# Kernel optimization log

Measured on AMD Instinct MI355X. Metric: run time of the kernel, lower is better.

Reference implementation:

```python
import jax, jax.numpy as jnp
import numpy as np

B, S, E, H = 4, 2048, 256, 8  # batch, seq_len, embed_dim, depth (heads)


def setup_inputs() -> dict:
    key = jax.random.key(0)
    k_x, k_q, k_k, k_v = jax.random.split(key, 4)
    return {
        "x": jax.random.normal(k_x, (B, S, E), dtype=jnp.float32),
        "w_q": jax.random.normal(k_q, (H, E, E), dtype=jnp.float32),
        "w_k": jax.random.normal(k_k, (H, E, E), dtype=jnp.float32),
        "w_v": jax.random.normal(k_v, (H, E, E), dtype=jnp.float32),
    }


def reference(x, w_q, w_k, w_v):
    # Each head uses full embed_dim projections; heads are averaged at the end.
    embed_dim = x.shape[-1]
    scale = 1.0 / np.sqrt(embed_dim).astype(np.float32)
    q = jnp.einsum("bse,hef->bhsf", x, w_q)  # [B,H,S,E]
    k = jnp.einsum("bse,hef->bhsf", x, w_k)
    v = jnp.einsum("bse,hef->bhsf", x, w_v)
    scores = jax.nn.softmax(jnp.einsum("bhsf,bhtf->bhst", q, k) * scale, axis=-1)
    out = jnp.einsum("bhst,bhtf->bhsf", scores, v)  # [B,H,S,E]
    return out.mean(axis=1)  # [B,S,E]
```

## Files before the change

kernel.cpp:

```cpp
#include <hip/hip_runtime.h>
#include <hip/hip_bf16.h>
#include <cstdint>

#define B_N 4
#define S_N 2048
#define E_N 256
#define H_N 8

typedef float f32x4 __attribute__((ext_vector_type(4)));
typedef int i32x4 __attribute__((ext_vector_type(4)));
typedef short s16x8 __attribute__((ext_vector_type(8)));

static __device__ __forceinline__ f32x4 mfma16(s16x8 a, s16x8 b, f32x4 c) {
  return __builtin_amdgcn_mfma_f32_16x16x32_bf16(a, b, c, 0, 0, 0);
}
static __device__ __forceinline__ i32x4 mfma8i(i32x4 a, i32x4 b, i32x4 c) {
  return __builtin_amdgcn_mfma_i32_16x16x64_i8(a, b, c, 0, 0, 0);
}

static __device__ __forceinline__ unsigned short f2bf(float f) {
  union { float f; unsigned int u; } v; v.f = f;
  unsigned int r = v.u + 0x7fffu + ((v.u >> 16) & 1u);
  return (unsigned short)(r >> 16);
}
static __device__ __forceinline__ float bf2f(unsigned short s) {
  union { unsigned int u; float f; } v; v.u = ((unsigned int)s) << 16;
  return v.f;
}
static __device__ __forceinline__ unsigned short f2bf_fast(float f) {
  __hip_bfloat16 h = __float2bfloat16(f);
  return *(unsigned short*)&h;
}

static __device__ __forceinline__ void limbs(float v, float scale, int& hi8, int& lo8) {
  int x = (int)lrintf(v * scale);
  x = x < -32639 ? -32639 : (x > 32639 ? 32639 : x);
  hi8 = (x + 128) >> 8;
  lo8 = x - (hi8 << 8);
}

static __device__ __forceinline__ void gload16(const void* g, void* l) {
  __builtin_amdgcn_global_load_lds(
      (const __attribute__((address_space(1))) unsigned int*)g,
      (__attribute__((address_space(3))) unsigned int*)l, 16, 0, 0);
}

static __device__ __forceinline__ float dppmax16(float x) {
  x = fmaxf(x, __int_as_float(__builtin_amdgcn_update_dpp(
          0, __float_as_int(x), 0xB1, 0xF, 0xF, true)));
  x = fmaxf(x, __int_as_float(__builtin_amdgcn_update_dpp(
          0, __float_as_int(x), 0x4E, 0xF, 0xF, true)));
  x = fmaxf(x, __int_as_float(__builtin_amdgcn_update_dpp(
          0, __float_as_int(x), 0x141, 0xF, 0xF, true)));
  x = fmaxf(x, __int_as_float(__builtin_amdgcn_update_dpp(
          0, __float_as_int(x), 0x140, 0xF, 0xF, true)));
  return x;
}
static __device__ __forceinline__ float dppsum16(float x) {
  x = x + __int_as_float(__builtin_amdgcn_update_dpp(
          0, __float_as_int(x), 0xB1, 0xF, 0xF, true));
  x = x + __int_as_float(__builtin_amdgcn_update_dpp(
          0, __float_as_int(x), 0x4E, 0xF, 0xF, true));
  x = x + __int_as_float(__builtin_amdgcn_update_dpp(
          0, __float_as_int(x), 0x141, 0xF, 0xF, true));
  x = x + __int_as_float(__builtin_amdgcn_update_dpp(
          0, __float_as_int(x), 0x140, 0xF, 0xF, true));
  return x;
}

__global__ void k_split(const float* __restrict__ src, unsigned short* __restrict__ hi,
                        unsigned short* __restrict__ lo, int n4) {
  int i = blockIdx.x * blockDim.x + threadIdx.x;
  if (i >= n4) return;
  float4 v = ((const float4*)src)[i];
  float f[4] = {v.x, v.y, v.z, v.w};
  unsigned short hh[4], ll[4];
#pragma unroll
  for (int j = 0; j < 4; j++) {
    hh[j] = f2bf(f[j]);
    ll[j] = f2bf(f[j] - bf2f(hh[j]));
  }
  ushort4 h; h.x = hh[0]; h.y = hh[1]; h.z = hh[2]; h.w = hh[3];
  ushort4 l; l.x = ll[0]; l.y = ll[1]; l.z = ll[2]; l.w = ll[3];
  ((ushort4*)hi)[i] = h;
  ((ushort4*)lo)[i] = l;
}

__global__ void k_split8(const float* __restrict__ src, signed char* __restrict__ hi,
                         signed char* __restrict__ lo, int n4) {
  int i = blockIdx.x * blockDim.x + threadIdx.x;
  if (i >= n4) return;
  float4 v = ((const float4*)src)[i];
  float f[4] = {v.x, v.y, v.z, v.w};
  signed char hh[4], ll[4];
#pragma unroll
  for (int j = 0; j < 4; j++) {
    int h8, l8;
    limbs(f[j], 4096.f, h8, l8);
    hh[j] = (signed char)h8;
    ll[j] = (signed char)l8;
  }
  *(int*)(hi + i * 4) = *(int*)hh;
  *(int*)(lo + i * 4) = *(int*)ll;
}

__global__ void k_transpose_wv(const float* __restrict__ wv, unsigned short* __restrict__ wvT) {
  __shared__ float t[32][33];
  int h = blockIdx.z;
  int e0 = blockIdx.x * 32, f0 = blockIdx.y * 32;
  int tx = threadIdx.x & 31, ty = threadIdx.x >> 5;
  const float* src = wv + ((size_t)h * E_N + e0) * E_N + f0;
#pragma unroll
  for (int r = ty; r < 32; r += 8) t[r][tx] = src[(size_t)r * E_N + tx];
  __syncthreads();
  unsigned short* dst = wvT + ((size_t)h * E_N + f0) * E_N + e0;
#pragma unroll
  for (int r = ty; r < 32; r += 8) dst[(size_t)r * E_N + tx] = f2bf(t[tx][r]);
}

#define BKP 40

template <int TERMS, int OUT_MODE>
__global__ __launch_bounds__(256, 2) void k_gemm(
    const unsigned short* __restrict__ Ahi, const unsigned short* __restrict__ Alo,
    const unsigned short* __restrict__ Bhi, const unsigned short* __restrict__ Blo,
    unsigned short* __restrict__ Chi, unsigned short* __restrict__ Clo,
    int K, int N,
    int aDiv, int aMod, long long aStr,
    int bDiv, int bMod, long long bStr,
    long long cStr) {
  __shared__ unsigned short sA[2][128 * BKP];
  __shared__ unsigned short sB[2][128 * BKP];
  int z = blockIdx.z;
  const unsigned short* A0h = Ahi + (long long)((z / aDiv) % aMod) * aStr;
  const unsigned short* A0l = Alo + (long long)((z / aDiv) % aMod) * aStr;
  const unsigned short* B0h = Bhi + (long long)((z / bDiv) % bMod) * bStr;
  const unsigned short* B0l = Blo + (long long)((z / bDiv) % bMod) * bStr;
  int rT = blockIdx.x * 128, cT = blockIdx.y * 128;
  int tid = threadIdx.x;
  int w = tid >> 6, l = tid & 63, lr = l & 15, lg = l >> 4;
  int wr = w >> 1, wc = w & 1;

  f32x4 acc[4][4];
#pragma unroll
  for (int i = 0; i < 4; i++)
#pragma unroll
    for (int j = 0; j < 4; j++) acc[i][j] = (f32x4){0.f, 0.f, 0.f, 0.f};

  for (int k0 = 0; k0 < K; k0 += 32) {
#pragma unroll
    for (int it = 0; it < 2; it++) {
      int idx = (it * 256 + tid) * 8;
      int r = idx >> 5, c = idx & 31;
      *(s16x8*)&sA[0][r * BKP + c] = *(const s16x8*)(A0h + (size_t)(rT + r) * K + k0 + c);
      *(s16x8*)&sB[0][r * BKP + c] = *(const s16x8*)(B0h + (size_t)(cT + r) * K + k0 + c);
      if (TERMS == 3) {
        *(s16x8*)&sA[1][r * BKP + c] = *(const s16x8*)(A0l + (size_t)(rT + r) * K + k0 + c);
        *(s16x8*)&sB[1][r * BKP + c] = *(const s16x8*)(B0l + (size_t)(cT + r) * K + k0 + c);
      }
    }
    __syncthreads();
    s16x8 ah[4], al[4], bh[4], bl[4];
#pragma unroll
    for (int i = 0; i < 4; i++) {
      ah[i] = *(const s16x8*)&sA[0][(wr * 64 + i * 16 + lr) * BKP + lg * 8];
      if (TERMS == 3) al[i] = *(const s16x8*)&sA[1][(wr * 64 + i * 16 + lr) * BKP + lg * 8];
    }
#pragma unroll
    for (int j = 0; j < 4; j++) {
      bh[j] = *(const s16x8*)&sB[0][(wc * 64 + j * 16 + lr) * BKP + lg * 8];
      if (TERMS == 3) bl[j] = *(const s16x8*)&sB[1][(wc * 64 + j * 16 + lr) * BKP + lg * 8];
    }
#pragma unroll
    for (int i = 0; i < 4; i++)
#pragma unroll
      for (int j = 0; j < 4; j++) {
        acc[i][j] = mfma16(ah[i], bh[j], acc[i][j]);
        if (TERMS == 3) {
          acc[i][j] = mfma16(ah[i], bl[j], acc[i][j]);
          acc[i][j] = mfma16(al[i], bh[j], acc[i][j]);
        }
      }
    __syncthreads();
  }
  long long cOff = (long long)z * cStr;
#pragma unroll
  for (int i = 0; i < 4; i++)
#pragma unroll
    for (int j = 0; j < 4; j++)
#pragma unroll
      for (int r = 0; r < 4; r++) {
        int row = rT + wr * 64 + i * 16 + lg * 4 + r;
        int col = cT + wc * 64 + j * 16 + lr;
        float v = acc[i][j][r];
        long long e = cOff + (size_t)row * N + col;
        if (OUT_MODE == 2) {
          int h8, l8;
          limbs(v, 16.f, h8, l8);
          ((signed char*)Chi)[e] = (signed char)h8;
          ((signed char*)Clo)[e] = (signed char)l8;
        } else {
          unsigned short hb = f2bf(v);
          Chi[e] = hb;
          if (OUT_MODE == 1) Clo[e] = f2bf(v - bf2f(hb));
        }
      }
}

#define TT 64
#define BUFS 65536
#define ATTN_LDS 147456
#define THR 40.f

__global__ __launch_bounds__(512, 2) void k_attn(
    const signed char* __restrict__ Y8h, const signed char* __restrict__ Y8l,
    const signed char* __restrict__ X8h, const signed char* __restrict__ X8l,
    const unsigned short* __restrict__ VT, float* __restrict__ Out) {
  extern __shared__ char smem[];

  int obid = blockIdx.x;
  int swz = (obid & 7) * 64 + (obid >> 3);
  int qt = swz & 15, bh = swz >> 4;
  int b = bh >> 3;
  int tid = threadIdx.x, w = tid >> 6, l = tid & 63, lr = l & 15, lg = l >> 4;
  const signed char* Ybh_h = Y8h + (size_t)bh * (S_N * E_N);
  const signed char* Ybh_l = Y8l + (size_t)bh * (S_N * E_N);
  const signed char* Xb_h = X8h + (size_t)b * (S_N * E_N);
  const signed char* Xb_l = X8l + (size_t)b * (S_N * E_N);
  const unsigned short* Vbh = VT + (size_t)bh * (E_N * S_N);
  int qrow = qt * 128 + w * 16;

  int xs8[2];
#pragma unroll
  for (int i = 0; i < 2; i++) {
    int c = (w * 2 + i) * 64 + l;
    int t8 = c >> 4;
    xs8[i] = t8 * 256 + (((c & 15) ^ (t8 & 15)) * 16);
  }
  int vsrc[4];
#pragma unroll
  for (int i = 0; i < 4; i++) {
    int c = (w * 4 + i) * 64 + l;
    int vrow = c >> 3, vbyt = (c & 7) * 16;
    vsrc[i] = vrow * S_N + ((vbyt ^ ((vrow & 7) << 4)) >> 1);
  }

  int xrb[4];
#pragma unroll
  for (int kb = 0; kb < 4; kb++)
    xrb[kb] = lr * 256 + (((kb * 4 + lg) ^ lr) * 16);
  int vtb[2];
#pragma unroll
  for (int tc = 0; tc < 2; tc++)
    vtb[tc] = lr * 128 + ((tc * 64 + lg * 16) ^ ((lr & 7) << 4));
  int prb = 131072 + w * 2048 + lr * 128 + ((lg * 16) ^ (((lr >> 2) & 3) << 4));
  int pwb = 131072 + w * 2048 + lg * 512;

  i32x4 yh8[4], yl8[4];
#pragma unroll
  for (int kb = 0; kb < 4; kb++) {
    yh8[kb] = *(const i32x4*)(Ybh_h + (size_t)(qrow + lr) * E_N + kb * 64 + lg * 16);
    yl8[kb] = *(const i32x4*)(Ybh_l + (size_t)(qrow + lr) * E_N + kb * 64 + lg * 16);
  }
  f32x4 o[16];
#pragma unroll
  for (int i = 0; i < 16; i++) o[i] = (f32x4){0.f, 0.f, 0.f, 0.f};
  float m2[4], lv[4];
#pragma unroll
  for (int r = 0; r < 4; r++) { m2[r] = -3.0e38f; lv[r] = 0.f; }

  const float C2T = 1.3758611398590895e-6f;

#pragma unroll
  for (int i = 0; i < 2; i++) {
    gload16(Xb_h + xs8[i], smem + (w * 2 + i) * 1024);
    gload16(Xb_l + xs8[i], smem + 16384 + (w * 2 + i) * 1024);
  }
#pragma unroll
  for (int i = 0; i < 4; i++)
    gload16(Vbh + vsrc[i], smem + 32768 + (w * 4 + i) * 1024);

#define TILE_BODY(CB, NB, t)                                                   \
  {                                                                            \
    asm volatile("s_waitcnt vmcnt(0)" ::: "memory");                           \
    __builtin_amdgcn_s_barrier();                                              \
    if ((t) < 31) {                                                            \
      _Pragma("unroll") for (int i = 0; i < 2; i++) {                          \
        gload16(Xb_h + (size_t)((t) + 1) * (TT * E_N) + xs8[i],                \
                smem + (NB) + (w * 2 + i) * 1024);                             \
        gload16(Xb_l + (size_t)((t) + 1) * (TT * E_N) + xs8[i],                \
                smem + (NB) + 16384 + (w * 2 + i) * 1024);                     \
      }                                                                        \
      _Pragma("unroll") for (int i = 0; i < 4; i++)                            \
          gload16(Vbh + ((t) + 1) * TT + vsrc[i],                              \
                  smem + (NB) + 32768 + (w * 4 + i) * 1024);                   \
    }                                                                          \
    f32x4 sc[4];                                                               \
    __builtin_amdgcn_s_setprio(1);                                             \
    _Pragma("unroll") for (int jp = 0; jp < 4; jp += 2) {                      \
      i32x4 i0[2], i1[2], i2[2];                                               \
      _Pragma("unroll") for (int u = 0; u < 2; u++) {                          \
        i0[u] = (i32x4){0, 0, 0, 0};                                           \
        i1[u] = (i32x4){0, 0, 0, 0};                                           \
        i2[u] = (i32x4){0, 0, 0, 0};                                           \
      }                                                                        \
      _Pragma("unroll") for (int u = 0; u < 2; u++) {                          \
        _Pragma("unroll") for (int kb = 0; kb < 4; kb++) {                     \
          i32x4 bh_ = *(const i32x4*)(smem + (CB) + (jp + u) * 4096 + xrb[kb]);\
          i32x4 bl_ =                                                          \
              *(const i32x4*)(smem + (CB) + 16384 + (jp + u) * 4096 + xrb[kb]);\
          i0[u] = mfma8i(yh8[kb], bh_, i0[u]);                                 \
          i1[u] = mfma8i(yh8[kb], bl_, i1[u]);                                 \
          i1[u] = mfma8i(yl8[kb], bh_, i1[u]);                                 \
          i2[u] = mfma8i(yl8[kb], bl_, i2[u]);                                 \
        }                                                                      \
      }                                                                        \
      _Pragma("unroll") for (int u = 0; u < 2; u++)                            \
          _Pragma("unroll") for (int r = 0; r < 4; r++)                        \
              sc[jp + u][r] = fmaf(65536.f, (float)i0[u][r],                   \
                                   fmaf(256.f, (float)i1[u][r],                \
                                        (float)i2[u][r]));                     \
    }                                                                          \
    __builtin_amdgcn_s_setprio(0);                                             \
    float t2[4];                                                               \
    _Pragma("unroll") for (int r = 0; r < 4; r++)                              \
        t2[r] = fmaxf(fmaxf(sc[0][r], sc[1][r]),                               \
                      fmaxf(sc[2][r], sc[3][r])) * C2T;                        \
    bool ok = (t2[0] <= m2[0] + THR) && (t2[1] <= m2[1] + THR) &&              \
              (t2[2] <= m2[2] + THR) && (t2[3] <= m2[3] + THR);                \
    if (!__all(ok)) {                                                          \
      float fr[4];                                                             \
      _Pragma("unroll") for (int r = 0; r < 4; r++) {                          \
        float rm = dppmax16(t2[r]);                                            \
        float nm = fmaxf(m2[r], rm);                                           \
        fr[r] = exp2f(m2[r] - nm);                                             \
        m2[r] = nm;                                                            \
        lv[r] *= fr[r];                                                        \
      }                                                                        \
      _Pragma("unroll") for (int i = 0; i < 16; i++)                           \
          _Pragma("unroll") for (int r = 0; r < 4; r++) o[i][r] *= fr[r];      \
    }                                                                          \
    float p[4][4];                                                             \
    _Pragma("unroll") for (int j = 0; j < 4; j++)                              \
        _Pragma("unroll") for (int r = 0; r < 4; r++)                          \
            p[j][r] = exp2f(fmaf(sc[j][r], C2T, -m2[r]));                      \
    _Pragma("unroll") for (int r = 0; r < 4; r++)                              \
        lv[r] += (p[0][r] + p[1][r]) + (p[2][r] + p[3][r]);                    \
    _Pragma("unroll") for (int j = 0; j < 4; j++)                              \
        _Pragma("unroll") for (int r = 0; r < 4; r++) {                        \
      int byt = (32 * j + 2 * lr) ^ (lg << 4);                                 \
      *(unsigned short*)(smem + pwb + r * 128 + byt) = f2bf_fast(p[j][r]);     \
    }                                                                          \
    __builtin_amdgcn_s_setprio(1);                                             \
    _Pragma("unroll") for (int tc = 0; tc < 2; tc++) {                         \
      s16x8 pa = *(const s16x8*)(smem + prb + tc * 64);                        \
      _Pragma("unroll") for (int jf = 0; jf < 16; jf++) {                      \
        s16x8 bv =                                                             \
            *(const s16x8*)(smem + (CB) + 32768 + vtb[tc] + jf * 2048);        \
        o[jf] = mfma16(pa, bv, o[jf]);                                         \
      }                                                                        \
    }                                                                          \
    __builtin_amdgcn_s_setprio(0);                                             \
  }

  for (int kt = 0; kt < S_N / TT; kt += 2) {
    TILE_BODY(0, BUFS, kt);
    TILE_BODY(BUFS, 0, kt + 1);
  }
#undef TILE_BODY

#pragma unroll
  for (int r = 0; r < 4; r++) lv[r] = dppsum16(lv[r]);
#pragma unroll
  for (int jf = 0; jf < 16; jf++)
#pragma unroll
    for (int r = 0; r < 4; r++) {
      float v = o[jf][r] / lv[r] * 0.125f;
      atomicAdd(&Out[((size_t)b * S_N + qrow + lg * 4 + r) * E_N + jf * 16 + lr], v);
    }
}

extern "C" void kernel_launch(void* const* d_in, const int* in_sizes, int n_in,
                              void* d_out, int out_size, void* d_ws, size_t ws_size,
                              hipStream_t stream) {
  const float* x = (const float*)d_in[0];
  const float* wq = (const float*)d_in[1];
  const float* wk = (const float*)d_in[2];
  const float* wv = (const float*)d_in[3];
  float* out = (float*)d_out;

  unsigned short* ws = (unsigned short*)d_ws;
  unsigned short* x_hi = ws;
  unsigned short* x_lo = x_hi + 2097152;
  unsigned short* wq_hi = x_lo + 2097152;
  unsigned short* wq_lo = wq_hi + 524288;
  unsigned short* wk_hi = wq_lo + 524288;
  unsigned short* wk_lo = wk_hi + 524288;
  unsigned short* wvT = wk_lo + 524288;
  unsigned short* mt_hi = wvT + 524288;
  unsigned short* mt_lo = mt_hi + 524288;
  unsigned short* vt = mt_lo + 524288;
  signed char* i8base = (signed char*)(vt + 16777216);
  signed char* y8h = i8base;
  signed char* y8l = y8h + 16777216;
  signed char* x8h = y8l + 16777216;
  signed char* x8l = x8h + 2097152;

  hipMemsetAsync(d_out, 0, (size_t)out_size * sizeof(float), stream);

  k_split<<<2048, 256, 0, stream>>>(x, x_hi, x_lo, 524288);
  k_split<<<512, 256, 0, stream>>>(wq, wq_hi, wq_lo, 131072);
  k_split<<<512, 256, 0, stream>>>(wk, wk_hi, wk_lo, 131072);
  k_split8<<<2048, 256, 0, stream>>>(x, x8h, x8l, 524288);
  k_transpose_wv<<<dim3(8, 8, 8), 256, 0, stream>>>(wv, wvT);

  k_gemm<3, 1><<<dim3(2, 2, 8), 256, 0, stream>>>(
      wk_hi, wk_lo, wq_hi, wq_lo, mt_hi, mt_lo, 256, 256,
      1, 8, 65536LL, 1, 8, 65536LL, 65536LL);
  k_gemm<3, 2><<<dim3(16, 2, 32), 256, 0, stream>>>(
      x_hi, x_lo, mt_hi, mt_lo, (unsigned short*)y8h, (unsigned short*)y8l,
      256, 256, 8, 4, 524288LL, 1, 8, 65536LL, 524288LL);
  k_gemm<1, 0><<<dim3(2, 16, 32), 256, 0, stream>>>(
      wvT, wvT, x_hi, x_hi, vt, vt, 256, 2048,
      1, 8, 65536LL, 8, 4, 524288LL, 524288LL);

  hipFuncSetAttribute((const void*)k_attn, hipFuncAttributeMaxDynamicSharedMemorySize,
                      ATTN_LDS);
  k_attn<<<dim3(512), 512, ATTN_LDS, stream>>>(y8h, y8l, x8h, x8l, vt, out);
}
```

Measured before the change: 342.7 us.

## Repartition PV matmul so each wave owns output columns across all query rows

The P·V stage changes from each wave computing all 256 output columns for its own 16 query rows to each wave computing 32 output columns for all 128 query rows of the block. The V fragments are then loaded once per wave and reused across 8 query groups, while P fragments are read from LDS for all waves. Rescale factors and row sums are exchanged through new LDS slots, and an extra workgroup barrier is added per tile to synchronise them. The aim is to cut redundant LDS reads of V, at the cost of an extra barrier per tile and cross-wave coupling of the online-softmax rescaling.

```diff
diff --git a/kernel.cpp b/kernel.cpp
--- a/kernel.cpp
+++ b/kernel.cpp
@@ -209,7 +209,10 @@
 
 #define TT 64
 #define BUFS 65536
-#define ATTN_LDS 147456
+#define FRB 147456
+#define FLB 147968
+#define LVB 148480
+#define ATTN_LDS 148992
 #define THR 40.f
 
 __global__ __launch_bounds__(512, 2) void k_attn(
@@ -253,7 +256,7 @@
 #pragma unroll
   for (int tc = 0; tc < 2; tc++)
     vtb[tc] = lr * 128 + ((tc * 64 + lg * 16) ^ ((lr & 7) << 4));
-  int prb = 131072 + w * 2048 + lr * 128 + ((lg * 16) ^ (((lr >> 2) & 3) << 4));
+  int prbB = 131072 + lr * 128 + ((lg * 16) ^ (((lr >> 2) & 3) << 4));
   int pwb = 131072 + w * 2048 + lg * 512;
 
   i32x4 yh8[4], yl8[4];
@@ -328,8 +331,9 @@
                       fmaxf(sc[2][r], sc[3][r])) * C2T;                        \
     bool ok = (t2[0] <= m2[0] + THR) && (t2[1] <= m2[1] + THR) &&              \
               (t2[2] <= m2[2] + THR) && (t2[3] <= m2[3] + THR);                \
-    if (!__all(ok)) {                                                          \
-      float fr[4];                                                             \
+    bool fired = !__all(ok);                                                   \
+    float fr[4];                                                               \
+    if (fired) {                                                               \
       _Pragma("unroll") for (int r = 0; r < 4; r++) {                          \
         float rm = dppmax16(t2[r]);                                            \
         float nm = fmaxf(m2[r], rm);                                           \
@@ -337,9 +341,14 @@
         m2[r] = nm;                                                            \
         lv[r] *= fr[r];                                                        \
       }                                                                        \
-      _Pragma("unroll") for (int i = 0; i < 16; i++)                           \
-          _Pragma("unroll") for (int r = 0; r < 4; r++) o[i][r] *= fr[r];      \
-    }                                                                          \
+    } else {                                                                   \
+      _Pragma("unroll") for (int r = 0; r < 4; r++) fr[r] = 1.f;               \
+    }                                                                          \
+    if ((l & 15) == 0) {                                                       \
+      _Pragma("unroll") for (int r = 0; r < 4; r++)                            \
+          *(float*)(smem + FRB + (w * 16 + lg * 4 + r) * 4) = fr[r];           \
+    }                                                                          \
+    if (l == 0) *(int*)(smem + FLB + w * 4) = fired ? 1 : 0;                   \
     float p[4][4];                                                             \
     _Pragma("unroll") for (int j = 0; j < 4; j++)                              \
         _Pragma("unroll") for (int r = 0; r < 4; r++)                          \
@@ -351,13 +360,28 @@
       int byt = (32 * j + 2 * lr) ^ (lg << 4);                                 \
       *(unsigned short*)(smem + pwb + r * 128 + byt) = f2bf_fast(p[j][r]);     \
     }                                                                          \
+    __builtin_amdgcn_s_barrier();                \
+    i32x4 fA = *(const i32x4*)(smem + FLB);                                    \
+    i32x4 fB = *(const i32x4*)(smem + FLB + 16);                               \
+    int anyf = fA[0] | fA[1] | fA[2] | fA[3] | fB[0] | fB[1] | fB[2] | fB[3];  \
+    if (anyf) {                                                                \
+      _Pragma("unroll") for (int qg = 0; qg < 8; qg++)                         \
+          _Pragma("unroll") for (int r = 0; r < 4; r++) {                      \
+        float ff = *(const float*)(smem + FRB + (qg * 16 + lg * 4 + r) * 4);   \
+        o[qg * 2][r] *= ff;                                                    \
+        o[qg * 2 + 1][r] *= ff;                                                \
+      }                                                                        \
+    }                                                                          \
     __builtin_amdgcn_s_setprio(1);                                             \
     _Pragma("unroll") for (int tc = 0; tc < 2; tc++) {                         \
-      s16x8 pa = *(const s16x8*)(smem + prb + tc * 64);                        \
-      _Pragma("unroll") for (int jf = 0; jf < 16; jf++) {                      \
-        s16x8 bv =                                                             \
-            *(const s16x8*)(smem + (CB) + 32768 + vtb[tc] + jf * 2048);        \
-        o[jf] = mfma16(pa, bv, o[jf]);                                         \
+      s16x8 bv0 =                                                              \
+          *(const s16x8*)(smem + (CB) + 32768 + vtb[tc] + (w * 2) * 2048);     \
+      s16x8 bv1 =                                                              \
+          *(const s16x8*)(smem + (CB) + 32768 + vtb[tc] + (w * 2 + 1) * 2048); \
+      _Pragma("unroll") for (int qg = 0; qg < 8; qg++) {                       \
+        s16x8 pa = *(const s16x8*)(smem + prbB + qg * 2048 + tc * 64);         \
+        o[qg * 2] = mfma16(pa, bv0, o[qg * 2]);                                \
+        o[qg * 2 + 1] = mfma16(pa, bv1, o[qg * 2 + 1]);                        \
       }                                                                        \
     }                                                                          \
     __builtin_amdgcn_s_setprio(0);                                             \
@@ -371,12 +395,23 @@
 
 #pragma unroll
   for (int r = 0; r < 4; r++) lv[r] = dppsum16(lv[r]);
-#pragma unroll
-  for (int jf = 0; jf < 16; jf++)
+  __builtin_amdgcn_s_barrier();
+  if ((l & 15) == 0) {
+#pragma unroll
+    for (int r = 0; r < 4; r++)
+      *(float*)(smem + LVB + (w * 16 + lg * 4 + r) * 4) = lv[r];
+  }
+  __builtin_amdgcn_s_barrier();
+  int qbase = qt * 128;
+#pragma unroll
+  for (int qg = 0; qg < 8; qg++)
 #pragma unroll
     for (int r = 0; r < 4; r++) {
-      float v = o[jf][r] / lv[r] * 0.125f;
-      atomicAdd(&Out[((size_t)b * S_N + qrow + lg * 4 + r) * E_N + jf * 16 + lr], v);
+      float lvv = *(const float*)(smem + LVB + (qg * 16 + lg * 4 + r) * 4);
+      float inv = 0.125f / lvv;
+      size_t row = (size_t)b * S_N + qbase + qg * 16 + lg * 4 + r;
+      atomicAdd(&Out[row * E_N + (w * 2) * 16 + lr], o[qg * 2][r] * inv);
+      atomicAdd(&Out[row * E_N + (w * 2 + 1) * 16 + lr], o[qg * 2 + 1][r] * inv);
     }
 }
 
```

New measurement: 374.0 us. 9.1% more time.
